# Optimization experiments

Hardware: AMD Instinct MI355X
Metric: run time of the kernel (lower is better)

Reference implementation:

```python
import jax, jax.numpy as jnp
import numpy as np

NUM_BINS = 256


def setup_inputs() -> dict:
    key = jax.random.key(0)
    # pixel intensities uniform in [0, 256) -> populates all 256 bins
    img = jax.random.uniform(key, (16, 2048, 2048), dtype=jnp.float32) * NUM_BINS
    return {"img": img}


def reference(img):
    # Faithful to DE3.forward: for each batch element the original loops over
    # 256 bins, counting (img < i+1) & (img >= i) over the ENTIRE tensor (not
    # img[b]) and dividing by temp = H*W. Since the inner computation does not
    # depend on b, the result is B * (8 - res) with res the "entropy" of the
    # full-tensor histogram normalized by H*W.
    B, H, W = img.shape
    temp = H * W
    # single-pass histogram: bin i counts values with floor(img) == i, i in [0,256)
    idx = jnp.floor(img).astype(jnp.int32)
    in_range = (img >= 0) & (img < NUM_BINS)
    idx = jnp.where(in_range, idx, NUM_BINS)  # out-of-range -> overflow bin
    counts = jnp.bincount(idx.ravel(), length=NUM_BINS + 1)[:NUM_BINS]  # [256]
    p = counts.astype(jnp.float32) / temp
    # res = -sum_{p_i > 0} p_i * log2(p_i)
    res = -jnp.sum(jnp.where(p > 0, p * jnp.log2(jnp.where(p > 0, p, 1.0)), 0.0))
    return B * (8.0 - res)
```

## Files before the change

### kernel.cpp

```cpp
#include <hip/hip_runtime.h>


#define NBINS 256
#define HIST_BLOCKS 2048
#define HIST_THREADS 256

__global__ void zero_hist(unsigned int* __restrict__ hist) {
    hist[threadIdx.x] = 0u;
}

__global__ __launch_bounds__(HIST_THREADS) void hist_kernel(
        const float* __restrict__ img,
        unsigned int* __restrict__ ghist,
        int n_vec4, long long n_total) {
    __shared__ unsigned int lhist[4][NBINS];
    const int wave = threadIdx.x >> 6;

    for (int i = threadIdx.x; i < 4 * NBINS; i += HIST_THREADS)
        ((unsigned int*)lhist)[i] = 0u;
    __syncthreads();

    const float4* __restrict__ img4 = (const float4*)img;
    const int tid = blockIdx.x * HIST_THREADS + threadIdx.x;
    const int stride = gridDim.x * HIST_THREADS;

    for (int i = tid; i < n_vec4; i += stride) {
        float4 v = img4[i];
        if (v.x >= 0.0f && v.x < 256.0f) atomicAdd(&lhist[wave][(int)v.x], 1u);
        if (v.y >= 0.0f && v.y < 256.0f) atomicAdd(&lhist[wave][(int)v.y], 1u);
        if (v.z >= 0.0f && v.z < 256.0f) atomicAdd(&lhist[wave][(int)v.z], 1u);
        if (v.w >= 0.0f && v.w < 256.0f) atomicAdd(&lhist[wave][(int)v.w], 1u);
    }
    for (long long j = 4LL * n_vec4 + tid; j < n_total; j += stride) {
        float v = img[j];
        if (v >= 0.0f && v < 256.0f) atomicAdd(&lhist[wave][(int)v], 1u);
    }

    __syncthreads();
    unsigned int s = lhist[0][threadIdx.x] + lhist[1][threadIdx.x] +
                     lhist[2][threadIdx.x] + lhist[3][threadIdx.x];
    if (s) atomicAdd(&ghist[threadIdx.x], s);
}

__global__ void entropy_kernel(const unsigned int* __restrict__ ghist,
                               float* __restrict__ out,
                               float B, float inv_temp) {
    const int t = threadIdx.x;
    unsigned int c = ghist[t];
    float term = 0.0f;
    if (c > 0u) {
        float p = (float)c * inv_temp;
        term = p * __log2f(p);
    }
    #pragma unroll
    for (int off = 32; off > 0; off >>= 1)
        term += __shfl_down(term, off, 64);
    __shared__ float wsum[4];
    if ((t & 63) == 0) wsum[t >> 6] = term;
    __syncthreads();
    if (t == 0) {
        float s = wsum[0] + wsum[1] + wsum[2] + wsum[3];
        out[0] = B * (8.0f + s);
    }
}

extern "C" void kernel_launch(void* const* d_in, const int* in_sizes, int n_in,
                              void* d_out, int out_size, void* d_ws, size_t ws_size,
                              hipStream_t stream) {
    const float* img = (const float*)d_in[0];
    float* out = (float*)d_out;
    unsigned int* ghist = (unsigned int*)d_ws;

    const long long n = (long long)in_sizes[0];
    const long long HW = 2048LL * 2048LL;
    const float B = (float)(n / HW);
    const float inv_temp = 1.0f / (float)HW;
    const int n_vec4 = (int)(n / 4);

    zero_hist<<<dim3(1), dim3(NBINS), 0, stream>>>(ghist);
    hist_kernel<<<dim3(HIST_BLOCKS), dim3(HIST_THREADS), 0, stream>>>(
        img, ghist, n_vec4, n);
    entropy_kernel<<<dim3(1), dim3(NBINS), 0, stream>>>(ghist, out, B, inv_temp);
}
```

Measured before the change: 367.1 us.

## Fuse entropy into histogram kernel via last-block ticket, unroll nontemporal loads

Folds the entropy reduction into the histogram kernel: each block bumps a ticket counter after flushing its shared histogram, and the last block to finish reads the global counts and computes the output. This removes one kernel launch. The main loop now issues two nontemporal 16-byte loads per iteration to keep more memory requests in flight. In exchange it adds a threadfence and a global atomic per block, and it relies on the ticket slot in the workspace being zeroed correctly.

```diff
diff --git a/kernel.cpp b/kernel.cpp
--- a/kernel.cpp
+++ b/kernel.cpp
@@ -5,31 +5,50 @@
 #define HIST_BLOCKS 2048
 #define HIST_THREADS 256
 
+typedef float f32x4 __attribute__((ext_vector_type(4)));
+
 __global__ void zero_hist(unsigned int* __restrict__ hist) {
     hist[threadIdx.x] = 0u;
+    if (threadIdx.x == 0) hist[NBINS] = 0u;
 }
 
-__global__ __launch_bounds__(HIST_THREADS) void hist_kernel(
+__global__ __launch_bounds__(HIST_THREADS) void hist_entropy_kernel(
         const float* __restrict__ img,
         unsigned int* __restrict__ ghist,
-        int n_vec4, long long n_total) {
+        float* __restrict__ out,
+        int n_vec4, long long n_total,
+        float B, float inv_temp) {
     __shared__ unsigned int lhist[4][NBINS];
-    const int wave = threadIdx.x >> 6;
+    const int t = threadIdx.x;
+    const int wave = t >> 6;
 
-    for (int i = threadIdx.x; i < 4 * NBINS; i += HIST_THREADS)
+    for (int i = t; i < 4 * NBINS; i += HIST_THREADS)
         ((unsigned int*)lhist)[i] = 0u;
     __syncthreads();
 
-    const float4* __restrict__ img4 = (const float4*)img;
-    const int tid = blockIdx.x * HIST_THREADS + threadIdx.x;
+    const f32x4* __restrict__ img4 = (const f32x4*)img;
+    const int tid = blockIdx.x * HIST_THREADS + t;
     const int stride = gridDim.x * HIST_THREADS;
 
-    for (int i = tid; i < n_vec4; i += stride) {
-        float4 v = img4[i];
-        if (v.x >= 0.0f && v.x < 256.0f) atomicAdd(&lhist[wave][(int)v.x], 1u);
-        if (v.y >= 0.0f && v.y < 256.0f) atomicAdd(&lhist[wave][(int)v.y], 1u);
-        if (v.z >= 0.0f && v.z < 256.0f) atomicAdd(&lhist[wave][(int)v.z], 1u);
-        if (v.w >= 0.0f && v.w < 256.0f) atomicAdd(&lhist[wave][(int)v.w], 1u);
+    int i = tid;
+    for (; i + stride < n_vec4; i += 2 * stride) {
+        f32x4 a = __builtin_nontemporal_load(&img4[i]);
+        f32x4 b = __builtin_nontemporal_load(&img4[i + stride]);
+        #pragma unroll
+        for (int k = 0; k < 4; ++k)
+            if (a[k] >= 0.0f && a[k] < 256.0f)
+                atomicAdd(&lhist[wave][(int)a[k]], 1u);
+        #pragma unroll
+        for (int k = 0; k < 4; ++k)
+            if (b[k] >= 0.0f && b[k] < 256.0f)
+                atomicAdd(&lhist[wave][(int)b[k]], 1u);
+    }
+    for (; i < n_vec4; i += stride) {
+        f32x4 a = __builtin_nontemporal_load(&img4[i]);
+        #pragma unroll
+        for (int k = 0; k < 4; ++k)
+            if (a[k] >= 0.0f && a[k] < 256.0f)
+                atomicAdd(&lhist[wave][(int)a[k]], 1u);
     }
     for (long long j = 4LL * n_vec4 + tid; j < n_total; j += stride) {
         float v = img[j];
@@ -37,30 +56,30 @@
     }
 
     __syncthreads();
-    unsigned int s = lhist[0][threadIdx.x] + lhist[1][threadIdx.x] +
-                     lhist[2][threadIdx.x] + lhist[3][threadIdx.x];
-    if (s) atomicAdd(&ghist[threadIdx.x], s);
-}
+    unsigned int s = lhist[0][t] + lhist[1][t] + lhist[2][t] + lhist[3][t];
+    if (s) atomicAdd(&ghist[t], s);
 
-__global__ void entropy_kernel(const unsigned int* __restrict__ ghist,
-                               float* __restrict__ out,
-                               float B, float inv_temp) {
-    const int t = threadIdx.x;
-    unsigned int c = ghist[t];
-    float term = 0.0f;
-    if (c > 0u) {
-        float p = (float)c * inv_temp;
-        term = p * __log2f(p);
-    }
-    #pragma unroll
-    for (int off = 32; off > 0; off >>= 1)
-        term += __shfl_down(term, off, 64);
-    __shared__ float wsum[4];
-    if ((t & 63) == 0) wsum[t >> 6] = term;
+    __threadfence();
+    __shared__ unsigned int ticket;
+    if (t == 0) ticket = atomicAdd(&ghist[NBINS], 1u);
     __syncthreads();
-    if (t == 0) {
-        float s = wsum[0] + wsum[1] + wsum[2] + wsum[3];
-        out[0] = B * (8.0f + s);
+    if (ticket == (unsigned int)(gridDim.x - 1)) {
+        unsigned int c = atomicAdd(&ghist[t], 0u);
+        float term = 0.0f;
+        if (c > 0u) {
+            float p = (float)c * inv_temp;
+            term = p * __log2f(p);
+        }
+        #pragma unroll
+        for (int off = 32; off > 0; off >>= 1)
+            term += __shfl_down(term, off, 64);
+        __shared__ float wsum[4];
+        if ((t & 63) == 0) wsum[t >> 6] = term;
+        __syncthreads();
+        if (t == 0) {
+            float ssum = wsum[0] + wsum[1] + wsum[2] + wsum[3];
+            out[0] = B * (8.0f + ssum);
+        }
     }
 }
 
@@ -78,7 +97,6 @@
     const int n_vec4 = (int)(n / 4);
 
     zero_hist<<<dim3(1), dim3(NBINS), 0, stream>>>(ghist);
-    hist_kernel<<<dim3(HIST_BLOCKS), dim3(HIST_THREADS), 0, stream>>>(
-        img, ghist, n_vec4, n);
-    entropy_kernel<<<dim3(1), dim3(NBINS), 0, stream>>>(ghist, out, B, inv_temp);
+    hist_entropy_kernel<<<dim3(HIST_BLOCKS), dim3(HIST_THREADS), 0, stream>>>(
+        img, ghist, out, n_vec4, n, B, inv_temp);
 }
```

Result: slower. 576.3 us (+57.0%).
